# Performance work log

Measured on AMD Instinct MI355X. Metric: run time of the kernel, lower is better.

## Reference

```python
import jax, jax.numpy as jnp
import numpy as np

V, E, H, B, S, T = 32000, 512, 1024, 32, 64, 64

def setup_inputs() -> dict:
    key = jax.random.key(0)
    ks = jax.random.split(key, 26)
    p = 0.02  # param init scale
    inp = {
        "enc_h": jax.random.normal(ks[0], (B, S, 2 * H), dtype=jnp.float32),
        "prev_s": jax.random.normal(ks[1], (B, H), dtype=jnp.float32),
        "target": jax.random.randint(ks[2], (B, T), 0, V, dtype=jnp.int32),
        "embed": jax.random.normal(ks[3], (V, E), dtype=jnp.float32) * p,
        # Attention params
        "att_Wenc": jax.random.normal(ks[4], (2 * H, H), dtype=jnp.float32) * p,
        "att_benc": jnp.zeros((H,), dtype=jnp.float32),
        "att_Wprev": jax.random.normal(ks[5], (H, H), dtype=jnp.float32) * p,
        "att_bprev": jnp.zeros((H,), dtype=jnp.float32),
        "att_wlin": jax.random.normal(ks[6], (H, 1), dtype=jnp.float32) * p,
        "att_blin": jnp.zeros((1,), dtype=jnp.float32),
        # DecoderCell gate params (input/hidden/ctx -> 2H)
        "dc_Wi": jax.random.normal(ks[7], (E, 2 * H), dtype=jnp.float32) * p,
        "dc_bi": jnp.zeros((2 * H,), dtype=jnp.float32),
        "dc_Wh": jax.random.normal(ks[8], (H, 2 * H), dtype=jnp.float32) * p,
        "dc_bh": jnp.zeros((2 * H,), dtype=jnp.float32),
        "dc_Wc": jax.random.normal(ks[9], (2 * H, 2 * H), dtype=jnp.float32) * p,
        "dc_bc": jnp.zeros((2 * H,), dtype=jnp.float32),
        # DecoderCell candidate params (-> H)
        "dc_Wi2": jax.random.normal(ks[10], (E, H), dtype=jnp.float32) * p,
        "dc_bi2": jnp.zeros((H,), dtype=jnp.float32),
        "dc_Wh2": jax.random.normal(ks[11], (H, H), dtype=jnp.float32) * p,
        "dc_bh2": jnp.zeros((H,), dtype=jnp.float32),
        "dc_Wc2": jax.random.normal(ks[12], (2 * H, H), dtype=jnp.float32) * p,
        "dc_bc2": jnp.zeros((H,), dtype=jnp.float32),
        # dec2word
        "out_W": jax.random.normal(ks[13], (H, V), dtype=jnp.float32) * p,
        "out_b": jnp.zeros((V,), dtype=jnp.float32),
    }
    return inp


def reference(enc_h, prev_s, target, embed, att_Wenc, att_benc, att_Wprev,
              att_bprev, att_wlin, att_blin, dc_Wi, dc_bi, dc_Wh, dc_bh,
              dc_Wc, dc_bc, dc_Wi2, dc_bi2, dc_Wh2, dc_bh2, dc_Wc2, dc_bc2,
              out_W, out_b):
    h = prev_s.shape[-1]
    # Precompute attention key projection (weights fixed across timesteps)
    enc_proj = enc_h @ att_Wenc + att_benc          # B x S x H
    xs = jnp.transpose(embed[target], (1, 0, 2))    # T x B x E

    def step(s_prev, x_t):
        # Bahdanau attention
        q = s_prev @ att_Wprev + att_bprev                       # B x H
        score = jnp.tanh(enc_proj + q[:, None, :]) @ att_wlin + att_blin  # B x S x 1
        alpha = jax.nn.softmax(score[..., 0], axis=1)            # B x S (over seq)
        ctx = jnp.einsum('bs,bsh->bh', alpha, enc_h)             # B x 2H
        # GRU-like cell (original uses only the first chunk of gates)
        gates = (x_t @ dc_Wi + dc_bi) + (s_prev @ dc_Wh + dc_bh) + (ctx @ dc_Wc + dc_bc)
        reset = jax.nn.sigmoid(gates[:, :h])
        s_tilde = jnp.tanh((x_t @ dc_Wi2 + dc_bi2) + (s_prev @ dc_Wh2 + dc_bh2) + (ctx @ dc_Wc2 + dc_bc2))
        s_new = (1.0 - reset) * s_prev + reset * s_tilde
        return s_new, s_new

    final_s, dec_h = jax.lax.scan(step, prev_s, xs)   # dec_h: T x B x H
    outputs = jnp.transpose(dec_h, (1, 0, 2)) @ out_W + out_b  # B x T x V
    return outputs, final_s
```

## Files before the change

### kernel.cpp

```cpp
#include <hip/hip_runtime.h>

#define B_   32
#define S_   64
#define T_   64
#define H_   1024
#define H2_  2048
#define E_   512
#define V_   32000
#define K3_  3072
#define BT_  2048

typedef unsigned short u16;
typedef __attribute__((ext_vector_type(8))) short short8_t;
typedef __attribute__((ext_vector_type(4))) float f32x4;

__device__ __forceinline__ u16 f2bf(float f) {
  unsigned x = __float_as_uint(f);
  unsigned r = (x + 0x7fffu + ((x >> 16) & 1u)) >> 16;
  return (u16)r;
}
__device__ __forceinline__ float bf2f(u16 h) {
  return __uint_as_float(((unsigned)h) << 16);
}
__device__ __forceinline__ float frcp(float x) { return __builtin_amdgcn_rcpf(x); }
__device__ __forceinline__ float ftanh(float x) {
  float e = __expf(2.f * x);
  return 1.f - 2.f * frcp(e + 1.f);
}
__device__ __forceinline__ float fsigm(float x) {
  return frcp(1.f + __expf(-x));
}

#define KEEPV(x) asm volatile("" : "+v"(x))

__device__ __forceinline__ void st_u16(u16* p, u16 v) {
  __hip_atomic_store(p, v, __ATOMIC_RELAXED, __HIP_MEMORY_SCOPE_AGENT);
}
__device__ __forceinline__ void st_f32(float* p, float v) {
  __hip_atomic_store(p, v, __ATOMIC_RELAXED, __HIP_MEMORY_SCOPE_AGENT);
}

#define MB_ (1ull << 20)
#define KB_ (1ull << 10)
#define X_OFF    (0)
#define XGR_OFF  (4*MB_)
#define XG2_OFF  (12*MB_)
#define ENCT_OFF (20*MB_)
#define QFV_OFF  (20*MB_)
#define WQF_OFF  (28*MB_)
#define WGF_OFF  (30*MB_)
#define XSV_OFF  (28*MB_)
#define XCV_OFF  (36*MB_)
#define WOT_OFF  (0)
#define DECH_OFF (54*MB_)
#define XS0_OFF  (58*MB_)
#define BAS_OFF  (58*MB_ + 128*KB_)
#define BCR_OFF  (58*MB_ + 132*KB_)
#define BC2_OFF  (58*MB_ + 136*KB_)
#define WLB_OFF  (58*MB_ + 140*KB_)
#define BAR_OFF  (58*MB_ + 144*KB_)

__device__ __forceinline__ u16* xs_hi(char* w, int t) {
  return (u16*)(t == 0 ? (w + XS0_OFF) : (w + XSV_OFF + (size_t)(t - 1) * 131072));
}
__device__ __forceinline__ u16* xc_hi(char* w, int t) {
  return (u16*)(w + XCV_OFF + (size_t)t * 262144);
}
__device__ __forceinline__ float* qf_v(char* w, int t) {
  return (float*)(w + QFV_OFF + (size_t)t * 131072);
}


__global__ void k_gather(float* __restrict__ x, const float* __restrict__ embed,
                         const int* __restrict__ tgt) {
  int bid = blockIdx.x;
  int t = bid >> 5, b = bid & 31;
  int row = tgt[b * T_ + t];
  const float4* src = (const float4*)(embed + (size_t)row * E_);
  float4* dst = (float4*)(x + (size_t)bid * E_);
  dst[threadIdx.x] = src[threadIdx.x];
}

__global__ void k_biascomb(float* bcr, float* bc2o, float* bas, u16* wlb,
                           const float* bi, const float* bh, const float* bc,
                           const float* bi2, const float* bh2, const float* bc2i,
                           const float* benc, const float* bprev, const float* wlin) {
  int j = blockIdx.x * 256 + threadIdx.x;
  if (j < H_) {
    bcr[j]  = bi[j]  + bh[j]  + bc[j];
    bc2o[j] = bi2[j] + bh2[j] + bc2i[j];
    bas[j]  = benc[j] + bprev[j];
    wlb[j]  = f2bf(wlin[j]);
  }
}

__global__ __launch_bounds__(256) void k_gemm(
    const float* __restrict__ A, int lda,
    const float* __restrict__ Bm, int ldb,
    void* __restrict__ Cv, int ldc, int outBf16,
    const float* __restrict__ bias,
    int mtiles, int ntiles, int K) {
  __shared__ u16 As[128][72];
  __shared__ u16 Bs[128][72];
  int nwg = mtiles * ntiles;
  int bid = blockIdx.x;
  int cpx = nwg >> 3;
  int lb = (bid & 7) * cpx + (bid >> 3);
  int ntb = lb / mtiles, mtb = lb - ntb * mtiles;
  size_t m0 = (size_t)mtb * 128, n0 = (size_t)ntb * 128;
  int t = threadIdx.x, lane = t & 63, wid = t >> 6;
  int wr = (wid >> 1) * 64, wc = (wid & 1) * 64;
  f32x4 acc[4][4] = {};
  for (int k0 = 0; k0 < K; k0 += 64) {
    #pragma unroll
    for (int i = 0; i < 8; ++i) {
      int f4 = i * 256 + t;
      int row = f4 >> 4, c4 = (f4 & 15) << 2;
      float4 v = *(const float4*)(A + (m0 + row) * (size_t)lda + k0 + c4);
      ushort4 u; u.x = f2bf(v.x); u.y = f2bf(v.y); u.z = f2bf(v.z); u.w = f2bf(v.w);
      *(ushort4*)&As[row][c4] = u;
    }
    #pragma unroll
    for (int i = 0; i < 8; ++i) {
      int f4 = i * 256 + t;
      int kr = f4 >> 5, c4 = (f4 & 31) << 2;
      float4 v = *(const float4*)(Bm + (size_t)(k0 + kr) * ldb + n0 + c4);
      Bs[c4 + 0][kr] = f2bf(v.x);
      Bs[c4 + 1][kr] = f2bf(v.y);
      Bs[c4 + 2][kr] = f2bf(v.z);
      Bs[c4 + 3][kr] = f2bf(v.w);
    }
    __syncthreads();
    #pragma unroll
    for (int kk = 0; kk < 64; kk += 32) {
      int ko = kk + (lane >> 4) * 8;
      short8_t am[4], bn[4];
      #pragma unroll
      for (int m = 0; m < 4; ++m) am[m] = *(const short8_t*)&As[wr + m * 16 + (lane & 15)][ko];
      #pragma unroll
      for (int n = 0; n < 4; ++n) bn[n] = *(const short8_t*)&Bs[wc + n * 16 + (lane & 15)][ko];
      #pragma unroll
      for (int m = 0; m < 4; ++m)
        #pragma unroll
        for (int n = 0; n < 4; ++n)
          acc[m][n] = __builtin_amdgcn_mfma_f32_16x16x32_bf16(am[m], bn[n], acc[m][n], 0, 0, 0);
    }
    __syncthreads();
  }
  #pragma unroll
  for (int n = 0; n < 4; ++n) {
    int col = wc + n * 16 + (lane & 15);
    float bv = bias ? bias[n0 + col] : 0.f;
    #pragma unroll
    for (int m = 0; m < 4; ++m) {
      size_t row = m0 + wr + m * 16 + ((lane >> 4) << 2);
      #pragma unroll
      for (int r = 0; r < 4; ++r) {
        float val = acc[m][n][r] + bv;
        if (outBf16) ((u16*)Cv)[(row + r) * (size_t)ldc + n0 + col] = f2bf(val);
        else ((float*)Cv)[(row + r) * (size_t)ldc + n0 + col] = val;
      }
    }
  }
}

__global__ __launch_bounds__(256) void k_transE(u16* __restrict__ encT,
                                                const float* __restrict__ enc_h) {
  __shared__ u16 ld[64][68];
  int b = blockIdx.x >> 5, et = blockIdx.x & 31;
  int e0 = et * 64;
  int t = threadIdx.x;
  #pragma unroll
  for (int i = 0; i < 4; ++i) {
    int f4 = i * 256 + t;
    int si = f4 >> 4, e4 = (f4 & 15) << 2;
    float4 v = *(const float4*)(enc_h + ((size_t)(b * 64 + si)) * H2_ + e0 + e4);
    ld[si][e4 + 0] = f2bf(v.x); ld[si][e4 + 1] = f2bf(v.y);
    ld[si][e4 + 2] = f2bf(v.z); ld[si][e4 + 3] = f2bf(v.w);
  }
  __syncthreads();
  #pragma unroll
  for (int i = 0; i < 2; ++i) {
    int idx = i * 256 + t;
    int e = idx >> 3, s8 = (idx & 7) << 3;
    short8_t o;
    #pragma unroll
    for (int k = 0; k < 8; ++k) o[k] = (short)ld[s8 + k][e];
    *(short8_t*)(encT + ((size_t)(e0 + e)) * 2048 + b * 64 + s8) = o;
  }
}

__global__ __launch_bounds__(256) void k_packq(u16* __restrict__ wqf,
                                               const float* __restrict__ W) {
  __shared__ float ld[64][33];
  int jt = blockIdx.x & 31, kt = blockIdx.x >> 5;
  int c0 = jt * 32, k0 = kt * 64;
  int t = threadIdx.x;
  #pragma unroll
  for (int i = 0; i < 8; ++i) {
    int idx = i * 256 + t; int kr = idx >> 5, jc = idx & 31;
    ld[kr][jc] = W[(size_t)(k0 + kr) * H_ + c0 + jc];
  }
  __syncthreads();
  int u = t;
  int gl = u >> 7, kbl = (u >> 6) & 1, sub = (u >> 4) & 3, c = u & 15;
  int colLoc = gl * 16 + c;
  int gG = jt * 2 + gl, KB = kt * 2 + kbl;
  size_t lin = ((size_t)(gG * 32 + KB) * 4 + sub) * 16 + c;
  short8_t o;
  #pragma unroll
  for (int j = 0; j < 8; ++j) o[j] = (short)f2bf(ld[kbl * 32 + sub * 8 + j][colLoc]);
  *(short8_t*)(wqf + lin * 8) = o;
}

__global__ __launch_bounds__(256) void k_packg(
    u16* __restrict__ wgf, const float* __restrict__ Wh, const float* __restrict__ Wc,
    const float* __restrict__ Wh2, const float* __restrict__ Wc2) {
  __shared__ float ld[64][33];
  int sel = blockIdx.x & 1;
  int jt  = (blockIdx.x >> 1) & 31;
  int kt  = blockIdx.x >> 6;
  int k0 = kt * 64, j0 = jt * 32;
  int t = threadIdx.x;
  const float* srcW = (k0 < H_) ? (sel ? Wh2 : Wh) : (sel ? Wc2 : Wc);
  int ldw = sel ? H_ : H2_;
  int koff = (k0 < H_) ? k0 : (k0 - H_);
  #pragma unroll
  for (int i = 0; i < 8; ++i) {
    int idx = i * 256 + t; int kr = idx >> 5, jc = idx & 31;
    ld[kr][jc] = srcW[(size_t)(koff + kr) * ldw + j0 + jc];
  }
  __syncthreads();
  #pragma unroll
  for (int it = 0; it < 2; ++it) {
    int u = it * 256 + t;
    int m = u & 3, sub = (u >> 2) & 3, kbl = (u >> 4) & 1, islo = (u >> 5) & 1, gg = u >> 6;
    int jjLoc = gg * 4 + m;
    int p = 2 * (j0 + jjLoc) + sel;
    int g = p >> 3, cc = p & 7;
    int c = cc + 8 * islo;
    int KB = kt * 2 + kbl;
    size_t lin = ((size_t)(g * 96 + KB) * 4 + sub) * 16 + c;
    short8_t o;
    #pragma unroll
    for (int j = 0; j < 8; ++j) {
      float v = ld[kbl * 32 + sub * 8 + j][jjLoc];
      u16 h = f2bf(v);
      o[j] = (short)(islo ? f2bf(v - bf2f(h)) : h);
    }
    *(short8_t*)(wgf + lin * 8) = o;
  }
}

__global__ __launch_bounds__(256) void k_wtrans(u16* __restrict__ wot,
                                                const float* __restrict__ W, int nbase) {
  __shared__ u16 ld[64][68];
  int nt = blockIdx.x % 250, kt = blockIdx.x / 250;
  int n0 = nbase + nt * 64, k0 = kt * 64;
  int t = threadIdx.x;
  #pragma unroll
  for (int i = 0; i < 4; ++i) {
    int f4 = i * 256 + t;
    int kr = f4 >> 4, n4 = (f4 & 15) << 2;
    float4 v = *(const float4*)(W + (size_t)(k0 + kr) * V_ + n0 + n4);
    ld[kr][n4 + 0] = f2bf(v.x); ld[kr][n4 + 1] = f2bf(v.y);
    ld[kr][n4 + 2] = f2bf(v.z); ld[kr][n4 + 3] = f2bf(v.w);
  }
  __syncthreads();
  #pragma unroll
  for (int i = 0; i < 2; ++i) {
    int idx = i * 256 + t;
    int n = idx >> 3, k8 = (idx & 7) << 3;
    short8_t o;
    #pragma unroll
    for (int k = 0; k < 8; ++k) o[k] = (short)ld[k8 + k][n];
    *(short8_t*)(wot + ((size_t)(nt * 64 + n)) * H_ + k0 + k8) = o;
  }
}

__global__ __launch_bounds__(256) void k_gemm2(
    const u16* __restrict__ A, const u16* __restrict__ Bt,
    float* __restrict__ C, const float* __restrict__ bias, int n0g) {
  __shared__ u16 As[128][72];
  __shared__ u16 Bs[128][72];
  int bid = blockIdx.x;
  int lb = (bid & 7) * 250 + (bid >> 3);
  int mtb = lb & 15, ntb = lb >> 4;
  size_t m0 = (size_t)mtb * 128;
  size_t nl0 = (size_t)ntb * 128;
  int t = threadIdx.x, lane = t & 63, wid = t >> 6;
  int wr = (wid >> 1) * 64, wc = (wid & 1) * 64;
  f32x4 acc[4][4] = {};
  for (int k0 = 0; k0 < H_; k0 += 64) {
    #pragma unroll
    for (int i = 0; i < 4; ++i) {
      int idx = i * 256 + t;
      int row = idx >> 3, c8 = (idx & 7) << 3;
      *(short8_t*)&As[row][c8] = *(const short8_t*)(A + (m0 + row) * H_ + k0 + c8);
      *(short8_t*)&Bs[row][c8] = *(const short8_t*)(Bt + (nl0 + row) * H_ + k0 + c8);
    }
    __syncthreads();
    #pragma unroll
    for (int kk = 0; kk < 64; kk += 32) {
      int ko = kk + (lane >> 4) * 8;
      short8_t am[4], bn[4];
      #pragma unroll
      for (int m = 0; m < 4; ++m) am[m] = *(const short8_t*)&As[wr + m * 16 + (lane & 15)][ko];
      #pragma unroll
      for (int n = 0; n < 4; ++n) bn[n] = *(const short8_t*)&Bs[wc + n * 16 + (lane & 15)][ko];
      #pragma unroll
      for (int m = 0; m < 4; ++m)
        #pragma unroll
        for (int n = 0; n < 4; ++n)
          acc[m][n] = __builtin_amdgcn_mfma_f32_16x16x32_bf16(am[m], bn[n], acc[m][n], 0, 0, 0);
    }
    __syncthreads();
  }
  #pragma unroll
  for (int n = 0; n < 4; ++n) {
    int col = n0g + (int)nl0 + wc + n * 16 + (lane & 15);
    float bv = bias[col];
    #pragma unroll
    for (int m = 0; m < 4; ++m) {
      size_t row = m0 + wr + m * 16 + ((lane >> 4) << 2);
      #pragma unroll
      for (int r = 0; r < 4; ++r)
        C[(row + r) * (size_t)V_ + col] = acc[m][n][r] + bv;
    }
  }
}


__device__ __forceinline__ void gridbar(int* bar, int target) {
  asm volatile("s_waitcnt vmcnt(0)" ::: "memory");
  __syncthreads();
  if (threadIdx.x == 0) {
    int* leaf  = bar;
    int* root  = bar + 512;
    int* epoch = bar + 528;
    int li = (blockIdx.x >> 3) * 16;
    if (__hip_atomic_fetch_add(&leaf[li], 1, __ATOMIC_RELAXED, __HIP_MEMORY_SCOPE_AGENT) == 7) {
      __hip_atomic_store(&leaf[li], 0, __ATOMIC_RELAXED, __HIP_MEMORY_SCOPE_AGENT);
      if (__hip_atomic_fetch_add(root, 1, __ATOMIC_RELAXED, __HIP_MEMORY_SCOPE_AGENT) == 31) {
        __hip_atomic_store(root, 0, __ATOMIC_RELAXED, __HIP_MEMORY_SCOPE_AGENT);
        __hip_atomic_store(epoch, target, __ATOMIC_RELAXED, __HIP_MEMORY_SCOPE_AGENT);
      }
    }
    while (__hip_atomic_load(epoch, __ATOMIC_RELAXED, __HIP_MEMORY_SCOPE_AGENT) != target)
      __builtin_amdgcn_s_sleep(1);
  }
  __syncthreads();
}

#define MFMA16(a, b, c) __builtin_amdgcn_mfma_f32_16x16x32_bf16((a), (b), (c), 0, 0, 0)

__global__ __launch_bounds__(512, 2) void k_mega(
    char* w, u16* __restrict__ dech, float* __restrict__ fout,
    const u16* __restrict__ wqf, const u16* __restrict__ wgf,
    const u16* __restrict__ encp, const u16* __restrict__ encT,
    const float* __restrict__ xgr, const float* __restrict__ xg2,
    const float* __restrict__ prev_s, const u16* __restrict__ wlb,
    int* bar) {
  const int t = threadIdx.x, blk = blockIdx.x;
  const int lane = t & 63, wid = t >> 6;
  const int l15 = lane & 15, l4 = lane >> 4;
  const int klo = l4 * 8;
  __shared__ short8_t wg_lds[6144];
  __shared__ f32x4 scr[1024];
  __shared__ float sc[64];
  int ep = 0;

  for (int i = t; i < 6144; i += 512)
    wg_lds[i] = *(const short8_t*)(wgf + ((size_t)blk * 6144 + i) * 8);

  const int gq = blk & 63;
  short8_t wq[4];
  #pragma unroll
  for (int i = 0; i < 4; ++i) {
    wq[i] = *(const short8_t*)(wqf + ((size_t)(gq * 32 + wid * 4 + i) * 64 + lane) * 8);
    KEEPV(wq[i]);
  }
  const int bb = blk >> 3, eg = blk & 7;
  short8_t epv[8][2];
  #pragma unroll
  for (int r = 0; r < 8; ++r) {
    const u16* p = encp + ((size_t)(bb * 64 + wid * 8 + r)) * H_ + lane * 16;
    epv[r][0] = *(const short8_t*)(p);     KEEPV(epv[r][0]);
    epv[r][1] = *(const short8_t*)(p + 8); KEEPV(epv[r][1]);
  }
  short8_t wlv[2];
  wlv[0] = *(const short8_t*)(wlb + lane * 16);     KEEPV(wlv[0]);
  wlv[1] = *(const short8_t*)(wlb + lane * 16 + 8); KEEPV(wlv[1]);
  const int eloc = t >> 1, half = t & 1;
  const int ecol = eg * 256 + eloc;
  short8_t et[4];
  #pragma unroll
  for (int i = 0; i < 4; ++i) {
    et[i] = *(const short8_t*)(encT + (size_t)ecol * 2048 + bb * 64 + half * 32 + i * 8);
    KEEPV(et[i]);
  }

  const int pc4 = blk * 8 + l15, jcol = pc4 >> 1, isc = pc4 & 1;
  const int rb = wid * 16 + l4 * 4;
  const bool fin = (wid < 2) && (l15 < 8);
  float sreg[4] = {0.f, 0.f, 0.f, 0.f};

  {
    int idx = blk * 512 + t;
    u16* xs0h = xs_hi(w, 0);
    u16* xs0l = xs0h + B_ * H_;
    if (idx < B_ * H_) {
      float v = prev_s[idx];
      u16 h = f2bf(v);
      st_u16(&xs0h[idx], h);
      st_u16(&xs0l[idx], f2bf(v - bf2f(h)));
    }
    if (fin) {
      #pragma unroll
      for (int r = 0; r < 4; ++r) sreg[r] = prev_s[(rb + r) * H_ + jcol];
    }
  }
  gridbar(bar, ++ep);

  for (int ts = 0; ts < T_; ++ts) {
    const u16* xsh = xs_hi(w, ts);
    const u16* xsl = xsh + B_ * H_;
    u16* xch = xc_hi(w, ts);
    u16* xcl = xch + B_ * H2_;
    float* qfv = qf_v(w, ts);

    float xv[4] = {0.f, 0.f, 0.f, 0.f};
    if (fin) {
      const float* xg = isc ? xg2 : xgr;
      #pragma unroll
      for (int r = 0; r < 4; ++r)
        xv[r] = xg[((size_t)ts * B_ + rb + r) * H_ + jcol];
    }

    if (blk < 64) {
      f32x4 aA = {}, aB = {};
      #pragma unroll
      for (int i = 0; i < 4; ++i) {
        int kof = (wid * 4 + i) * 32 + klo;
        short8_t avA = *(const short8_t*)(xsh + l15 * H_ + kof);
        short8_t avB = *(const short8_t*)(xsh + (l15 + 16) * H_ + kof);
        aA = MFMA16(avA, wq[i], aA);
        aB = MFMA16(avB, wq[i], aB);
      }
      scr[(wid * 2 + 0) * 64 + lane] = aA;
      scr[(wid * 2 + 1) * 64 + lane] = aB;
      __syncthreads();
      if (wid < 2) {
        f32x4 s = scr[wid * 64 + lane];
        #pragma unroll
        for (int i = 1; i < 8; ++i) s += scr[(i * 2 + wid) * 64 + lane];
        int col = gq * 16 + l15;
        #pragma unroll
        for (int r = 0; r < 4; ++r)
          st_f32(&qfv[(size_t)(rb + r) * H_ + col], s[r]);
      }
    }
    gridbar(bar, ++ep);

    {
      float qv[16];
      #pragma unroll
      for (int i = 0; i < 4; ++i) {
        float4 s0 = *(const float4*)(qfv + (size_t)bb * H_ + lane * 16 + i * 4);
        qv[i * 4 + 0] = s0.x; qv[i * 4 + 1] = s0.y;
        qv[i * 4 + 2] = s0.z; qv[i * 4 + 3] = s0.w;
      }
      #pragma unroll
      for (int r = 0; r < 8; ++r) {
        float p = 0.f;
        #pragma unroll
        for (int jj = 0; jj < 16; ++jj)
          p += ftanh(bf2f((u16)epv[r][jj >> 3][jj & 7]) + qv[jj]) * bf2f((u16)wlv[jj >> 3][jj & 7]);
        #pragma unroll
        for (int off = 32; off; off >>= 1) p += __shfl_xor(p, off, 64);
        if (lane == 0) sc[wid * 8 + r] = p;
      }
      __syncthreads();
      if (wid == 0) {
        float v = sc[lane];
        float m = v;
        #pragma unroll
        for (int off = 32; off; off >>= 1) m = fmaxf(m, __shfl_xor(m, off, 64));
        float e = __expf(v - m);
        float s = e;
        #pragma unroll
        for (int off = 32; off; off >>= 1) s += __shfl_xor(s, off, 64);
        sc[lane] = e * frcp(s);
      }
      __syncthreads();
      {
        float a = 0.f;
        #pragma unroll
        for (int i = 0; i < 4; ++i)
          #pragma unroll
          for (int j = 0; j < 8; ++j)
            a += sc[half * 32 + i * 8 + j] * bf2f((u16)et[i][j]);
        a += __shfl_xor(a, 1, 64);
        if (half == 0) {
          u16 hh = f2bf(a);
          st_u16(&xch[bb * H2_ + ecol], hh);
          st_u16(&xcl[bb * H2_ + ecol], f2bf(a - bf2f(hh)));
        }
      }
    }
    gridbar(bar, ++ep);

    {
      f32x4 aA = {}, aB = {};
      #pragma unroll
      for (int i = 0; i < 12; ++i) {
        int kb = wid * 12 + i;
        int k = kb * 32 + klo;
        const u16 *ah, *al; int rs;
        if (kb < 32) { ah = xsh + l15 * H_ + k;          al = xsl + l15 * H_ + k;          rs = H_;  }
        else         { ah = xch + l15 * H2_ + (k - H_);  al = xcl + l15 * H2_ + (k - H_);  rs = H2_; }
        short8_t hA = *(const short8_t*)ah;
        short8_t lA = *(const short8_t*)al;
        short8_t hB = *(const short8_t*)(ah + 16 * rs);
        short8_t lB = *(const short8_t*)(al + 16 * rs);
        short8_t bv = wg_lds[kb * 64 + lane];
        aA = MFMA16(hA, bv, aA);
        aA = MFMA16(lA, bv, aA);
        aB = MFMA16(hB, bv, aB);
        aB = MFMA16(lB, bv, aB);
      }
      scr[(wid * 2 + 0) * 64 + lane] = aA;
      scr[(wid * 2 + 1) * 64 + lane] = aB;
      __syncthreads();
      if (wid < 2) {
        f32x4 s = scr[wid * 64 + lane];
        #pragma unroll
        for (int i = 1; i < 8; ++i) s += scr[(i * 2 + wid) * 64 + lane];
        float tot[4];
        #pragma unroll
        for (int r = 0; r < 4; ++r) tot[r] = s[r] + __shfl_xor(s[r], 8, 64);
        if (l15 < 8) {
          u16* nsh = xs_hi(w, ts + 1);
          u16* nsl = nsh + B_ * H_;
          #pragma unroll
          for (int r = 0; r < 4; ++r) {
            int brow = rb + r;
            float pre = tot[r] + xv[r];
            float mate = __shfl_xor(pre, 1, 64);
            float rpre = isc ? mate : pre;
            float cpre = isc ? pre : mate;
            float rg = fsigm(rpre);
            float cg = ftanh(cpre);
            float sp = sreg[r];
            float sn = sp + rg * (cg - sp);
            sreg[r] = sn;
            if (!isc) {
              u16 hh = f2bf(sn);
              st_u16(&nsh[brow * H_ + jcol], hh);
              st_u16(&nsl[brow * H_ + jcol], f2bf(sn - bf2f(hh)));
              dech[((size_t)brow * T_ + ts) * H_ + jcol] = hh;
              if (ts == T_ - 1) fout[brow * H_ + jcol] = sn;
            }
          }
        }
      }
    }
    gridbar(bar, ++ep);
  }
}


extern "C" void kernel_launch(void* const* d_in, const int* in_sizes, int n_in,
                              void* d_out, int out_size, void* d_ws, size_t ws_size,
                              hipStream_t stream) {
  const float* enc_h    = (const float*)d_in[0];
  const float* prev_s   = (const float*)d_in[1];
  const int*   target   = (const int*)d_in[2];
  const float* embed    = (const float*)d_in[3];
  const float* att_Wenc = (const float*)d_in[4];
  const float* att_benc = (const float*)d_in[5];
  const float* att_Wprev= (const float*)d_in[6];
  const float* att_bprev= (const float*)d_in[7];
  const float* att_wlin = (const float*)d_in[8];
  const float* dc_Wi    = (const float*)d_in[10];
  const float* dc_bi    = (const float*)d_in[11];
  const float* dc_Wh    = (const float*)d_in[12];
  const float* dc_bh    = (const float*)d_in[13];
  const float* dc_Wc    = (const float*)d_in[14];
  const float* dc_bc    = (const float*)d_in[15];
  const float* dc_Wi2   = (const float*)d_in[16];
  const float* dc_bi2   = (const float*)d_in[17];
  const float* dc_Wh2   = (const float*)d_in[18];
  const float* dc_bh2   = (const float*)d_in[19];
  const float* dc_Wc2   = (const float*)d_in[20];
  const float* dc_bc2   = (const float*)d_in[21];
  const float* out_W    = (const float*)d_in[22];
  const float* out_b    = (const float*)d_in[23];

  char* w = (char*)d_ws;
  float* x    = (float*)(w + X_OFF);
  float* xgr  = (float*)(w + XGR_OFF);
  float* xg2  = (float*)(w + XG2_OFF);
  u16*  encp  = (u16*)(w + X_OFF);
  u16*  encT  = (u16*)(w + ENCT_OFF);
  u16*  wqf   = (u16*)(w + WQF_OFF);
  u16*  wgf   = (u16*)(w + WGF_OFF);
  u16*  wot   = (u16*)(w + WOT_OFF);
  u16*  dech  = (u16*)(w + DECH_OFF);
  float* bas  = (float*)(w + BAS_OFF);
  float* bcr  = (float*)(w + BCR_OFF);
  float* bc2  = (float*)(w + BC2_OFF);
  u16*  wlb   = (u16*)(w + WLB_OFF);
  int*  bar   = (int*)(w + BAR_OFF);
  float* fout = (float*)d_out + (size_t)BT_ * V_;

  hipMemsetAsync(bar, 0, 4096, stream);

  k_gather  <<<BT_, 128, 0, stream>>>(x, embed, target);
  k_biascomb<<<4, 256, 0, stream>>>(bcr, bc2, bas, wlb,
                                    dc_bi, dc_bh, dc_bc, dc_bi2, dc_bh2, dc_bc2,
                                    att_benc, att_bprev, att_wlin);
  k_gemm<<<16 * 8, 256, 0, stream>>>(x, E_, dc_Wi,  H2_, xgr, H_, 0, bcr, 16, 8, E_);
  k_gemm<<<16 * 8, 256, 0, stream>>>(x, E_, dc_Wi2, H_,  xg2, H_, 0, bc2, 16, 8, E_);
  k_gemm<<<16 * 8, 256, 0, stream>>>(enc_h, H2_, att_Wenc, H_, encp, H_, 1, bas, 16, 8, H2_);
  k_transE<<<1024, 256, 0, stream>>>(encT, enc_h);
  k_packq <<<512, 256, 0, stream>>>(wqf, att_Wprev);
  k_packg <<<3072, 256, 0, stream>>>(wgf, dc_Wh, dc_Wc, dc_Wh2, dc_Wc2);

  k_mega<<<256, 512, 0, stream>>>(w, dech, fout,
                                  wqf, wgf, encp, encT, xgr, xg2,
                                  prev_s, wlb, bar);

  k_wtrans<<<4000, 256, 0, stream>>>(wot, out_W, 0);
  k_gemm2 <<<2000, 256, 0, stream>>>(dech, wot, (float*)d_out, out_b, 0);
  k_wtrans<<<4000, 256, 0, stream>>>(wot, out_W, 16000);
  k_gemm2 <<<2000, 256, 0, stream>>>(dech, wot, (float*)d_out, out_b, 16000);
}
```

Before: 3.459 ms.

## Use per-leaf epoch flags in grid barrier and prefetch state loads across it

The grid barrier now has the root block write the epoch into 32 separate per-leaf flags, so each group of eight blocks spins on its own cache line instead of all 256 blocks polling one epoch word. Each step also issues the hidden-state hi-part loads for the gate GEMM before the attention phase and barrier, so their latency overlaps that work. The K-block assignment per wave is interleaved (wid + 8*i) so those prefetched slices line up. Launch bounds drop to one block per CU, and the barrier memset grows to cover the new flags; the prefetch adds register pressure, and the root now does 32 stores per barrier.

```diff
diff --git a/kernel.cpp b/kernel.cpp
--- a/kernel.cpp
+++ b/kernel.cpp
@@ -335,26 +335,28 @@
   asm volatile("s_waitcnt vmcnt(0)" ::: "memory");
   __syncthreads();
   if (threadIdx.x == 0) {
-    int* leaf  = bar;
-    int* root  = bar + 512;
-    int* epoch = bar + 528;
-    int li = (blockIdx.x >> 3) * 16;
-    if (__hip_atomic_fetch_add(&leaf[li], 1, __ATOMIC_RELAXED, __HIP_MEMORY_SCOPE_AGENT) == 7) {
-      __hip_atomic_store(&leaf[li], 0, __ATOMIC_RELAXED, __HIP_MEMORY_SCOPE_AGENT);
+    int* leafcnt = bar;
+    int* root    = bar + 512;
+    int* leafep  = bar + 768;
+    int li = blockIdx.x >> 3;
+    if (__hip_atomic_fetch_add(&leafcnt[li * 16], 1, __ATOMIC_RELAXED, __HIP_MEMORY_SCOPE_AGENT) == 7) {
+      __hip_atomic_store(&leafcnt[li * 16], 0, __ATOMIC_RELAXED, __HIP_MEMORY_SCOPE_AGENT);
       if (__hip_atomic_fetch_add(root, 1, __ATOMIC_RELAXED, __HIP_MEMORY_SCOPE_AGENT) == 31) {
         __hip_atomic_store(root, 0, __ATOMIC_RELAXED, __HIP_MEMORY_SCOPE_AGENT);
-        __hip_atomic_store(epoch, target, __ATOMIC_RELAXED, __HIP_MEMORY_SCOPE_AGENT);
-      }
-    }
-    while (__hip_atomic_load(epoch, __ATOMIC_RELAXED, __HIP_MEMORY_SCOPE_AGENT) != target)
-      __builtin_amdgcn_s_sleep(1);
+        #pragma unroll
+        for (int i = 0; i < 32; ++i)
+          __hip_atomic_store(&leafep[i * 16], target, __ATOMIC_RELAXED, __HIP_MEMORY_SCOPE_AGENT);
+      }
+    }
+    while (__hip_atomic_load(&leafep[li * 16], __ATOMIC_RELAXED, __HIP_MEMORY_SCOPE_AGENT) != target)
+      __builtin_amdgcn_s_sleep(2);
   }
   __syncthreads();
 }
 
 #define MFMA16(a, b, c) __builtin_amdgcn_mfma_f32_16x16x32_bf16((a), (b), (c), 0, 0, 0)
 
-__global__ __launch_bounds__(512, 2) void k_mega(
+__global__ __launch_bounds__(512, 1) void k_mega(
     char* w, u16* __restrict__ dech, float* __restrict__ fout,
     const u16* __restrict__ wqf, const u16* __restrict__ wgf,
     const u16* __restrict__ encp, const u16* __restrict__ encT,
@@ -436,6 +438,13 @@
       for (int r = 0; r < 4; ++r)
         xv[r] = xg[((size_t)ts * B_ + rb + r) * H_ + jcol];
     }
+    short8_t pA[4], pB[4];
+    #pragma unroll
+    for (int i = 0; i < 4; ++i) {
+      int k = (wid + 8 * i) * 32 + klo;
+      pA[i] = *(const short8_t*)(xsh + l15 * H_ + k);        KEEPV(pA[i]);
+      pB[i] = *(const short8_t*)(xsh + (l15 + 16) * H_ + k); KEEPV(pB[i]);
+    }
 
     if (blk < 64) {
       f32x4 aA = {}, aB = {};
@@ -512,17 +521,33 @@
 
     {
       f32x4 aA = {}, aB = {};
-      #pragma unroll
-      for (int i = 0; i < 12; ++i) {
-        int kb = wid * 12 + i;
-        int k = kb * 32 + klo;
-        const u16 *ah, *al; int rs;
-        if (kb < 32) { ah = xsh + l15 * H_ + k;          al = xsl + l15 * H_ + k;          rs = H_;  }
-        else         { ah = xch + l15 * H2_ + (k - H_);  al = xcl + l15 * H2_ + (k - H_);  rs = H2_; }
-        short8_t hA = *(const short8_t*)ah;
-        short8_t lA = *(const short8_t*)al;
-        short8_t hB = *(const short8_t*)(ah + 16 * rs);
-        short8_t lB = *(const short8_t*)(al + 16 * rs);
+      short8_t loA[4], loB[4];
+      #pragma unroll
+      for (int i = 0; i < 4; ++i) {
+        int k = (wid + 8 * i) * 32 + klo;
+        loA[i] = *(const short8_t*)(xsl + l15 * H_ + k);
+        loB[i] = *(const short8_t*)(xsl + (l15 + 16) * H_ + k);
+      }
+      #pragma unroll
+      for (int i = 0; i < 4; ++i) {
+        short8_t bv = wg_lds[(wid + 8 * i) * 64 + lane];
+        aA = MFMA16(pA[i], bv, aA);
+        aB = MFMA16(pB[i], bv, aB);
+      }
+      #pragma unroll
+      for (int i = 0; i < 4; ++i) {
+        short8_t bv = wg_lds[(wid + 8 * i) * 64 + lane];
+        aA = MFMA16(loA[i], bv, aA);
+        aB = MFMA16(loB[i], bv, aB);
+      }
+      #pragma unroll
+      for (int i = 4; i < 12; ++i) {
+        int kb = wid + 8 * i;
+        int k = kb * 32 + klo - H_;
+        short8_t hA = *(const short8_t*)(xch + l15 * H2_ + k);
+        short8_t lA = *(const short8_t*)(xcl + l15 * H2_ + k);
+        short8_t hB = *(const short8_t*)(xch + (l15 + 16) * H2_ + k);
+        short8_t lB = *(const short8_t*)(xcl + (l15 + 16) * H2_ + k);
         short8_t bv = wg_lds[kb * 64 + lane];
         aA = MFMA16(hA, bv, aA);
         aA = MFMA16(lA, bv, aA);
@@ -614,7 +639,7 @@
   int*  bar   = (int*)(w + BAR_OFF);
   float* fout = (float*)d_out + (size_t)BT_ * V_;
 
-  hipMemsetAsync(bar, 0, 4096, stream);
+  hipMemsetAsync(bar, 0, 8192, stream);
 
   k_gather  <<<BT_, 128, 0, stream>>>(x, embed, target);
   k_biascomb<<<4, 256, 0, stream>>>(bcr, bc2, bas, wlb,
```

After: 3.188 ms. 7.8% less time.
